# Performance work log

Measured on AMD Instinct MI355X. Metric: run time of the kernel, lower is better.

Reference implementation:

```python
import jax, jax.numpy as jnp
import numpy as np

EPS = 1e-8
ACT_BITS = 8


def _ternary_vq(t):
    gamma = jnp.abs(t).mean()
    q = jnp.clip(jnp.round(t / (gamma + EPS)), -1.0, 1.0)
    return q * gamma


def setup_inputs() -> dict:
    key = jax.random.key(0)
    k1, k2, k3 = jax.random.split(key, 3)
    in_features, out_features = 1024, 1024
    x = jax.random.normal(k1, (8, 4096, in_features), dtype=jnp.float32)
    weight = jax.random.normal(k2, (out_features, in_features), dtype=jnp.float32)
    bias = jax.random.normal(k3, (out_features,), dtype=jnp.float32)
    return {"x": x, "weight": weight, "bias": bias}


def reference(x, weight, bias):
    # Weight/bias ternary quantization (done once in __init__ of the module)
    wq = _ternary_vq(weight)   # [out, in]
    bq = _ternary_vq(bias)     # [out]

    # Activation quantization: power-of-two scale from global absmax
    qmax = jnp.float32(2 ** (ACT_BITS - 1) - 1)  # 127
    max_val = jnp.max(jnp.abs(x))
    scale = jnp.exp2(jnp.floor(jnp.log2(max_val / qmax + EPS)))
    xq = jnp.round(jnp.clip(x, -qmax * scale, qmax * scale) / scale) * scale

    # F.linear: x @ W^T + b
    return jnp.einsum('bsi,oi->bso', xq, wq) + bq
```

## Files before the change

kernel.cpp:

```cpp
#include <hip/hip_runtime.h>

typedef __attribute__((ext_vector_type(4))) int int4v;

constexpr int Mdim = 32768;
constexpr int Kdim = 1024;
constexpr int Ndim = 1024;
constexpr float FEPS = 1e-8f;

constexpr size_t WQ_OFF = 32768;
constexpr size_t WS_NEED = WQ_OFF + (size_t)Ndim * Kdim;

__device__ __forceinline__ void gload16(const void* g, void* l) {
  __builtin_amdgcn_global_load_lds(
      (const __attribute__((address_space(1))) unsigned int*)g,
      (__attribute__((address_space(3))) unsigned int*)l, 16, 0, 0);
}

__global__ void k_pre(const uint4* __restrict__ xv, const float4* __restrict__ wv,
                      unsigned* __restrict__ pmax, float* __restrict__ partials) {
  const int tid = threadIdx.x;
  if (blockIdx.x < 2048) {
    int i0 = blockIdx.x * 256 + tid;
    const int stride = 2048 * 256;
    const int n4 = Mdim * Kdim / 4;
    unsigned m = 0u;
    for (int i = i0; i < n4; i += stride) {
      uint4 v = xv[i];
      m = max(m, v.x & 0x7fffffffu);
      m = max(m, v.y & 0x7fffffffu);
      m = max(m, v.z & 0x7fffffffu);
      m = max(m, v.w & 0x7fffffffu);
    }
    #pragma unroll
    for (int off = 32; off > 0; off >>= 1)
      m = max(m, (unsigned)__shfl_down((int)m, off, 64));
    __shared__ unsigned red[4];
    if ((tid & 63) == 0) red[tid >> 6] = m;
    __syncthreads();
    if (tid == 0)
      pmax[blockIdx.x] = max(max(red[0], red[1]), max(red[2], red[3]));
  } else {
    int wb = blockIdx.x - 2048;
    float s = 0.f;
    const int stride = 256 * 256;
    const int n4 = Ndim * Kdim / 4;
    for (int i = wb * 256 + tid; i < n4; i += stride) {
      float4 v = wv[i];
      s += fabsf(v.x) + fabsf(v.y) + fabsf(v.z) + fabsf(v.w);
    }
    __shared__ float red[256];
    red[tid] = s;
    __syncthreads();
    for (int h = 128; h > 0; h >>= 1) {
      if (tid < h) red[tid] += red[tid + h];
      __syncthreads();
    }
    if (tid == 0) partials[wb] = red[0];
  }
}

__global__ void k_finalize2(const float* __restrict__ bias, const float* __restrict__ w,
                            const float* __restrict__ partials, const unsigned* __restrict__ pmax,
                            float* __restrict__ scalars, float* __restrict__ bq,
                            unsigned char* __restrict__ wq) {
  __shared__ float red[256];
  const int t = threadIdx.x;
  const int b = blockIdx.x;

  red[t] = partials[t];
  __syncthreads();
  for (int h = 128; h > 0; h >>= 1) {
    if (t < h) red[t] += red[t + h];
    __syncthreads();
  }
  const float gw = red[0] / (1024.0f * 1024.0f);
  __syncthreads();
  const float inv_g = gw + FEPS;

  {
    const int tile = b * 4 + (t >> 6);
    const int nb = tile >> 4;
    const int kt = tile & 15;
    const int l = t & 63;
    const float4* src = (const float4*)(w + (size_t)(nb * 16 + (l >> 2)) * Kdim + kt * 64 + (l & 3) * 16);
    unsigned o[4];
    #pragma unroll
    for (int v = 0; v < 4; ++v) {
      float4 f = src[v];
      int a  = (int)rintf(fminf(fmaxf(f.x / inv_g, -1.f), 1.f));
      int bb = (int)rintf(fminf(fmaxf(f.y / inv_g, -1.f), 1.f));
      int cc = (int)rintf(fminf(fmaxf(f.z / inv_g, -1.f), 1.f));
      int dd = (int)rintf(fminf(fmaxf(f.w / inv_g, -1.f), 1.f));
      o[v] = (unsigned)(a & 0xff) | ((unsigned)(bb & 0xff) << 8) |
             ((unsigned)(cc & 0xff) << 16) | ((unsigned)(dd & 0xff) << 24);
    }
    uint4 pk; pk.x = o[0]; pk.y = o[1]; pk.z = o[2]; pk.w = o[3];
    const int lp = (l >> 2) | ((l & 3) << 4);
    *(uint4*)(wq + (size_t)tile * 1024 + lp * 16) = pk;
  }

  if (b != 0) return;

  __shared__ unsigned redu[256];
  __shared__ float sh_gb;
  unsigned m = 0u;
  #pragma unroll
  for (int i = 0; i < 8; ++i) m = max(m, pmax[t + 256 * i]);
  redu[t] = m;
  float s = fabsf(bias[t]) + fabsf(bias[t + 256]) + fabsf(bias[t + 512]) + fabsf(bias[t + 768]);
  red[t] = s;
  __syncthreads();
  for (int h = 128; h > 0; h >>= 1) {
    if (t < h) {
      red[t] += red[t + h];
      redu[t] = max(redu[t], redu[t + h]);
    }
    __syncthreads();
  }
  if (t == 0) {
    float gb = red[0] / 1024.0f;
    float maxval = __uint_as_float(redu[0]);
    float v = maxval / 127.0f + FEPS;
    int e = (int)((__float_as_uint(v) >> 23) & 0xff) - 127;
    float scale = ldexpf(1.0f, e);
    scalars[0] = gw;
    scalars[1] = gb;
    scalars[2] = scale;
    scalars[3] = scale * gw;
    scalars[4] = 127.0f * scale;
    scalars[5] = ldexpf(1.0f, -e);
    sh_gb = gb;
  }
  __syncthreads();
  float gb = sh_gb;
  for (int i = t; i < 1024; i += 256) {
    float q = rintf(bias[i] / (gb + FEPS));
    q = fminf(fmaxf(q, -1.0f), 1.0f);
    bq[i] = q * gb;
  }
}

__launch_bounds__(512, 4)
__global__ void k_megagemm(const float* __restrict__ x, const unsigned char* __restrict__ wq,
                           const float* __restrict__ scalars, const float* __restrict__ bq,
                           float* __restrict__ out) {
  __shared__ __align__(16) unsigned char lds[81920];
  unsigned char* Alds = lds;
  unsigned char* Bbuf = lds + 65536;

  const int tid = threadIdx.x;
  const int lane = tid & 63;
  const int wv = tid >> 6;
  const int mtile = blockIdx.x;
  const float qs = scalars[4], inv = scalars[5];

  #pragma unroll
  for (int i = 0; i < 8; ++i) {
    const int tile = wv * 8 + i;
    const int mb = tile >> 4;
    const int kt = tile & 15;
    const float4* src = (const float4*)(x + (size_t)(mtile * 64 + mb * 16 + (lane >> 2)) * Kdim
                                          + kt * 64 + (lane & 3) * 16);
    unsigned o[4];
    #pragma unroll
    for (int v = 0; v < 4; ++v) {
      float4 f = src[v];
      int a = (int)rintf(fminf(fmaxf(f.x, -qs), qs) * inv);
      int b = (int)rintf(fminf(fmaxf(f.y, -qs), qs) * inv);
      int c = (int)rintf(fminf(fmaxf(f.z, -qs), qs) * inv);
      int d = (int)rintf(fminf(fmaxf(f.w, -qs), qs) * inv);
      o[v] = (unsigned)(a & 0xff) | ((unsigned)(b & 0xff) << 8) |
             ((unsigned)(c & 0xff) << 16) | ((unsigned)(d & 0xff) << 24);
    }
    uint4 pk; pk.x = o[0]; pk.y = o[1]; pk.z = o[2]; pk.w = o[3];
    const int lp = (lane >> 2) | ((lane & 3) << 4);
    *(uint4*)(Alds + (size_t)tile * 1024 + lp * 16) = pk;
  }
  __syncthreads();

  const int wr = wv >> 2;
  const int wc = wv & 3;
  const float sg = scalars[3];
  const unsigned char* A0 = Alds + ((size_t)(wr * 2 + 0) * 16) * 1024 + lane * 16;
  const unsigned char* A1 = Alds + ((size_t)(wr * 2 + 1) * 16) * 1024 + lane * 16;

#define STAGEB(np_, kt_) \
    gload16(wq + ((size_t)(((np_) * 8 + wv) * 16 + (kt_))) * 1024 + lane * 16, \
            Bbuf + (((kt_) & 1) * 8192) + wv * 1024 + lane * 16)

  STAGEB(0, 0);

  #pragma unroll 1
  for (int np = 0; np < 8; ++np) {
    int4v acc[2][2];
    #pragma unroll
    for (int i = 0; i < 2; ++i)
      #pragma unroll
      for (int j = 0; j < 2; ++j)
        acc[i][j] = (int4v){0, 0, 0, 0};

    #pragma unroll
    for (int kt = 0; kt < 16; ++kt) {
      if (kt == 0) {
        if (np == 0) { asm volatile("s_waitcnt vmcnt(0)" ::: "memory"); }
        else         { asm volatile("s_waitcnt vmcnt(16)" ::: "memory"); }
      } else         { asm volatile("s_waitcnt vmcnt(0)" ::: "memory"); }
      __builtin_amdgcn_s_barrier();
      asm volatile("" ::: "memory");

      if (kt < 15) { STAGEB(np, kt + 1); }
      else if (np < 7) { STAGEB(np + 1, 0); }

      const unsigned char* bb = Bbuf + ((kt & 1) * 8192) + (size_t)(wc * 2) * 1024 + lane * 16;
      int4v b0 = *(const int4v*)(bb);
      int4v b1 = *(const int4v*)(bb + 1024);
      int4v a0 = *(const int4v*)(A0 + (size_t)kt * 1024);
      int4v a1 = *(const int4v*)(A1 + (size_t)kt * 1024);
      __builtin_amdgcn_s_setprio(1);
      acc[0][0] = __builtin_amdgcn_mfma_i32_16x16x64_i8(a0, b0, acc[0][0], 0, 0, 0);
      acc[0][1] = __builtin_amdgcn_mfma_i32_16x16x64_i8(a0, b1, acc[0][1], 0, 0, 0);
      acc[1][0] = __builtin_amdgcn_mfma_i32_16x16x64_i8(a1, b0, acc[1][0], 0, 0, 0);
      acc[1][1] = __builtin_amdgcn_mfma_i32_16x16x64_i8(a1, b1, acc[1][1], 0, 0, 0);
      __builtin_amdgcn_s_setprio(0);
    }

    #pragma unroll
    for (int nj = 0; nj < 2; ++nj) {
      const int col = np * 128 + (wc * 2 + nj) * 16 + (lane & 15);
      const float bb = bq[col];
      #pragma unroll
      for (int mi = 0; mi < 2; ++mi) {
        const int rowb = mtile * 64 + wr * 32 + mi * 16 + (lane >> 4) * 4;
        #pragma unroll
        for (int r = 0; r < 4; ++r)
          out[(size_t)(rowb + r) * Ndim + col] = (float)acc[mi][nj][r] * sg + bb;
      }
    }
  }
#undef STAGEB
}

extern "C" void kernel_launch(void* const* d_in, const int* in_sizes, int n_in,
                              void* d_out, int out_size, void* d_ws, size_t ws_size,
                              hipStream_t stream) {
  const float* x = (const float*)d_in[0];
  const float* weight = (const float*)d_in[1];
  const float* bias = (const float*)d_in[2];
  float* out = (float*)d_out;

  if (ws_size < WS_NEED) return;

  char* ws = (char*)d_ws;
  float* scalars = (float*)ws;
  float* partials = (float*)(ws + 1024);
  unsigned* pmax = (unsigned*)(ws + 4096);
  float* bq = (float*)(ws + 16384);
  unsigned char* wq = (unsigned char*)(ws + WQ_OFF);

  k_pre<<<2304, 256, 0, stream>>>((const uint4*)x, (const float4*)weight, pmax, partials);
  k_finalize2<<<256, 256, 0, stream>>>(bias, weight, partials, pmax, scalars, bq, wq);
  k_megagemm<<<512, 512, 0, stream>>>(x, wq, scalars, bq, out);
}
```

Baseline: 102.9 us.

## Load int8 weights directly into registers and widen per-wave tile to 64x32

The GEMM main loop no longer stages the ternary int8 weights through a double-buffered LDS ring with barriers. Each wave instead reads its B fragments straight from global memory into registers, prefetching one k-step ahead. Each wave now covers all 64 rows and 32 columns, using 8 accumulators and 4 column passes. This removes the per-k-step block barriers and frees 16KB of LDS. In exchange, A is read from LDS four times per k-step and B global-load latency is exposed with only shallow register prefetch.

Measured after the change: 303.3 us. +194.8%, slower.

```diff
diff --git a/kernel.cpp b/kernel.cpp
--- a/kernel.cpp
+++ b/kernel.cpp
@@ -9,12 +9,6 @@
 
 constexpr size_t WQ_OFF = 32768;
 constexpr size_t WS_NEED = WQ_OFF + (size_t)Ndim * Kdim;
-
-__device__ __forceinline__ void gload16(const void* g, void* l) {
-  __builtin_amdgcn_global_load_lds(
-      (const __attribute__((address_space(1))) unsigned int*)g,
-      (__attribute__((address_space(3))) unsigned int*)l, 16, 0, 0);
-}
 
 __global__ void k_pre(const uint4* __restrict__ xv, const float4* __restrict__ wv,
                       unsigned* __restrict__ pmax, float* __restrict__ partials) {
@@ -144,9 +138,7 @@
 __global__ void k_megagemm(const float* __restrict__ x, const unsigned char* __restrict__ wq,
                            const float* __restrict__ scalars, const float* __restrict__ bq,
                            float* __restrict__ out) {
-  __shared__ __align__(16) unsigned char lds[81920];
-  unsigned char* Alds = lds;
-  unsigned char* Bbuf = lds + 65536;
+  __shared__ __align__(16) unsigned char Alds[65536];
 
   const int tid = threadIdx.x;
   const int lane = tid & 63;
@@ -178,66 +170,80 @@
   }
   __syncthreads();
 
-  const int wr = wv >> 2;
-  const int wc = wv & 3;
   const float sg = scalars[3];
-  const unsigned char* A0 = Alds + ((size_t)(wr * 2 + 0) * 16) * 1024 + lane * 16;
-  const unsigned char* A1 = Alds + ((size_t)(wr * 2 + 1) * 16) * 1024 + lane * 16;
-
-#define STAGEB(np_, kt_) \
-    gload16(wq + ((size_t)(((np_) * 8 + wv) * 16 + (kt_))) * 1024 + lane * 16, \
-            Bbuf + (((kt_) & 1) * 8192) + wv * 1024 + lane * 16)
-
-  STAGEB(0, 0);
+  const unsigned char* A0 = Alds + lane * 16;
+  const unsigned char* A1 = Alds + 16 * 1024 + lane * 16;
+  const unsigned char* A2 = Alds + 32 * 1024 + lane * 16;
+  const unsigned char* A3 = Alds + 48 * 1024 + lane * 16;
+
+#define MF8(a0_, a1_, a2_, a3_, B0, B1) do {                                       \
+    acc[0][0] = __builtin_amdgcn_mfma_i32_16x16x64_i8(a0_, B0, acc[0][0], 0, 0, 0); \
+    acc[0][1] = __builtin_amdgcn_mfma_i32_16x16x64_i8(a0_, B1, acc[0][1], 0, 0, 0); \
+    acc[1][0] = __builtin_amdgcn_mfma_i32_16x16x64_i8(a1_, B0, acc[1][0], 0, 0, 0); \
+    acc[1][1] = __builtin_amdgcn_mfma_i32_16x16x64_i8(a1_, B1, acc[1][1], 0, 0, 0); \
+    acc[2][0] = __builtin_amdgcn_mfma_i32_16x16x64_i8(a2_, B0, acc[2][0], 0, 0, 0); \
+    acc[2][1] = __builtin_amdgcn_mfma_i32_16x16x64_i8(a2_, B1, acc[2][1], 0, 0, 0); \
+    acc[3][0] = __builtin_amdgcn_mfma_i32_16x16x64_i8(a3_, B0, acc[3][0], 0, 0, 0); \
+    acc[3][1] = __builtin_amdgcn_mfma_i32_16x16x64_i8(a3_, B1, acc[3][1], 0, 0, 0); \
+  } while (0)
 
   #pragma unroll 1
-  for (int np = 0; np < 8; ++np) {
-    int4v acc[2][2];
-    #pragma unroll
-    for (int i = 0; i < 2; ++i)
+  for (int np = 0; np < 4; ++np) {
+    int4v acc[4][2];
+    #pragma unroll
+    for (int i = 0; i < 4; ++i)
       #pragma unroll
       for (int j = 0; j < 2; ++j)
         acc[i][j] = (int4v){0, 0, 0, 0};
 
-    #pragma unroll
-    for (int kt = 0; kt < 16; ++kt) {
-      if (kt == 0) {
-        if (np == 0) { asm volatile("s_waitcnt vmcnt(0)" ::: "memory"); }
-        else         { asm volatile("s_waitcnt vmcnt(16)" ::: "memory"); }
-      } else         { asm volatile("s_waitcnt vmcnt(0)" ::: "memory"); }
-      __builtin_amdgcn_s_barrier();
-      asm volatile("" ::: "memory");
-
-      if (kt < 15) { STAGEB(np, kt + 1); }
-      else if (np < 7) { STAGEB(np + 1, 0); }
-
-      const unsigned char* bb = Bbuf + ((kt & 1) * 8192) + (size_t)(wc * 2) * 1024 + lane * 16;
-      int4v b0 = *(const int4v*)(bb);
-      int4v b1 = *(const int4v*)(bb + 1024);
+    const unsigned char* Bb = wq + ((size_t)(np * 16 + wv * 2) * 16) * 1024 + lane * 16;
+
+    int4v pb0, pb1, qb0, qb1;
+    pb0 = *(const int4v*)(Bb);
+    pb1 = *(const int4v*)(Bb + 16 * 1024);
+    qb0 = *(const int4v*)(Bb + 1024);
+    qb1 = *(const int4v*)(Bb + 16 * 1024 + 1024);
+
+    #pragma unroll
+    for (int kt = 0; kt < 16; kt += 2) {
       int4v a0 = *(const int4v*)(A0 + (size_t)kt * 1024);
       int4v a1 = *(const int4v*)(A1 + (size_t)kt * 1024);
+      int4v a2 = *(const int4v*)(A2 + (size_t)kt * 1024);
+      int4v a3 = *(const int4v*)(A3 + (size_t)kt * 1024);
       __builtin_amdgcn_s_setprio(1);
-      acc[0][0] = __builtin_amdgcn_mfma_i32_16x16x64_i8(a0, b0, acc[0][0], 0, 0, 0);
-      acc[0][1] = __builtin_amdgcn_mfma_i32_16x16x64_i8(a0, b1, acc[0][1], 0, 0, 0);
-      acc[1][0] = __builtin_amdgcn_mfma_i32_16x16x64_i8(a1, b0, acc[1][0], 0, 0, 0);
-      acc[1][1] = __builtin_amdgcn_mfma_i32_16x16x64_i8(a1, b1, acc[1][1], 0, 0, 0);
+      MF8(a0, a1, a2, a3, pb0, pb1);
       __builtin_amdgcn_s_setprio(0);
+      if (kt + 2 < 16) {
+        pb0 = *(const int4v*)(Bb + (size_t)(kt + 2) * 1024);
+        pb1 = *(const int4v*)(Bb + 16 * 1024 + (size_t)(kt + 2) * 1024);
+      }
+      int4v a4 = *(const int4v*)(A0 + (size_t)(kt + 1) * 1024);
+      int4v a5 = *(const int4v*)(A1 + (size_t)(kt + 1) * 1024);
+      int4v a6 = *(const int4v*)(A2 + (size_t)(kt + 1) * 1024);
+      int4v a7 = *(const int4v*)(A3 + (size_t)(kt + 1) * 1024);
+      __builtin_amdgcn_s_setprio(1);
+      MF8(a4, a5, a6, a7, qb0, qb1);
+      __builtin_amdgcn_s_setprio(0);
+      if (kt + 3 < 16) {
+        qb0 = *(const int4v*)(Bb + (size_t)(kt + 3) * 1024);
+        qb1 = *(const int4v*)(Bb + 16 * 1024 + (size_t)(kt + 3) * 1024);
+      }
     }
 
     #pragma unroll
     for (int nj = 0; nj < 2; ++nj) {
-      const int col = np * 128 + (wc * 2 + nj) * 16 + (lane & 15);
+      const int col = np * 256 + wv * 32 + nj * 16 + (lane & 15);
       const float bb = bq[col];
       #pragma unroll
-      for (int mi = 0; mi < 2; ++mi) {
-        const int rowb = mtile * 64 + wr * 32 + mi * 16 + (lane >> 4) * 4;
+      for (int mi = 0; mi < 4; ++mi) {
+        const int rowb = mtile * 64 + mi * 16 + (lane >> 4) * 4;
         #pragma unroll
         for (int r = 0; r < 4; ++r)
           out[(size_t)(rowb + r) * Ndim + col] = (float)acc[mi][nj][r] * sg + bb;
       }
     }
   }
-#undef STAGEB
+#undef MF8
 }
 
 extern "C" void kernel_launch(void* const* d_in, const int* in_sizes, int n_in,
```
